# Kernel optimization log

Measured on AMD Instinct MI355X. Metric: run time of the kernel, lower is better.

The kernel has to match this reference:

```python
import jax, jax.numpy as jnp
import numpy as np

N_VARS = 100
MAX_LAG = 10
HIDDEN = 64
E = N_VARS * MAX_LAG  # number of tiny expert MLPs
BATCH = 4096


def setup_inputs() -> dict:
    key = jax.random.key(0)
    k_x, k_w1, k_b1, k_w2, k_b2 = jax.random.split(key, 5)
    x = jax.random.normal(k_x, (BATCH, E), dtype=jnp.float32)
    # PyTorch Linear(1, H): weight [H,1] -> stacked as [E, H]; bias [E, H]
    lim1 = 1.0  # kaiming-uniform-ish bound for fan_in=1
    W1 = jax.random.uniform(k_w1, (E, HIDDEN), dtype=jnp.float32, minval=-lim1, maxval=lim1)
    b1 = jax.random.uniform(k_b1, (E, HIDDEN), dtype=jnp.float32, minval=-lim1, maxval=lim1)
    # Linear(H, n_vars): weight [n_vars,H] -> stacked as [E, H, n_vars]; bias [E, n_vars]
    lim2 = 1.0 / np.sqrt(HIDDEN)
    W2 = jax.random.uniform(k_w2, (E, HIDDEN, N_VARS), dtype=jnp.float32, minval=-lim2, maxval=lim2)
    b2 = jax.random.uniform(k_b2, (E, N_VARS), dtype=jnp.float32, minval=-lim2, maxval=lim2)
    return {"x": x, "W1": W1, "b1": b1, "W2": W2, "b2": b2}


def reference(x, W1, b1, W2, b2):
    # Fused form of: sum_i Linear2_i(relu(Linear1_i(x[:, i:i+1])))
    # h[b,e,h] = relu(x[b,e] * W1[e,h] + b1[e,h])
    h = jax.nn.relu(x[:, :, None] * W1[None, :, :] + b1[None, :, :])  # [B,E,H]
    # sum over experts folded into the contraction: out[b,v] = sum_e h[b,e,:] @ W2[e,:,v]
    out = jnp.einsum("beh,ehv->bv", h, W2) + jnp.sum(b2, axis=0)  # [B,n_vars]
    return out
```

## Files before the change

kernel.cpp:

```cpp
#include <hip/hip_runtime.h>
#include <hip/hip_bf16.h>

#define NV 100
#define HID 64
#define NE 1000
#define NB 4096
#define ESPLIT 32
#define BLOBU 3648
#define NVP 112

typedef __attribute__((ext_vector_type(8))) short short8;
typedef __attribute__((ext_vector_type(8))) unsigned short ushort8;
typedef __attribute__((ext_vector_type(4))) float f32x4;
typedef __attribute__((ext_vector_type(4))) unsigned u32x4;
typedef __attribute__((ext_vector_type(4))) unsigned short u16x4;

__device__ __align__(16) float g_bsum[NV];

__device__ __forceinline__ short cvtbf(float f) {
    return __builtin_bit_cast(short, (__bf16)f);
}
__device__ __forceinline__ unsigned short f2bf(float f) {
    return (unsigned short)__builtin_bit_cast(short, (__bf16)f);
}
__device__ __forceinline__ float bf2f(unsigned short s) {
    union { unsigned u; float f; } v; v.u = ((unsigned)s) << 16;
    return v.f;
}
__device__ __forceinline__ float bcast_lo(unsigned u) {
    union { unsigned u; float f; } v; v.u = u << 16; return v.f;
}
__device__ __forceinline__ float bcast_hi(unsigned u) {
    union { unsigned u; float f; } v; v.u = u & 0xffff0000u; return v.f;
}
__device__ __forceinline__ unsigned pkbf(float a, float b) {
    return (unsigned)f2bf(a) | ((unsigned)f2bf(b) << 16);
}

__device__ __host__ __forceinline__ void esplit_range(int ks, int* pe0, int* pne) {
    int e0 = (ks < 26) ? 32 * ks : 832 + 28 * (ks - 26);
    int ne = (ks < 26) ? 32 : 28;
    *pe0 = e0; *pne = ne;
}

__global__ void bias_kernel(const float* __restrict__ b2) {
    int v = blockIdx.x;
    float s = 0.f;
    for (int e = threadIdx.x; e < NE; e += 256)
        s += b2[e * NV + v];
    __shared__ float red[4];
    for (int off = 32; off; off >>= 1) s += __shfl_down(s, off, 64);
    if ((threadIdx.x & 63) == 0) red[threadIdx.x >> 6] = s;
    __syncthreads();
    if (threadIdx.x == 0) g_bsum[v] = red[0] + red[1] + red[2] + red[3];
}

__global__ void init_kernel(float* __restrict__ out) {
    int idx = blockIdx.x * 256 + threadIdx.x;
    if (idx < NB * NV) out[idx] = g_bsum[idx % NV];
}

__global__ void prepass5(const float* __restrict__ W2, const float* __restrict__ W1,
                         const float* __restrict__ b1, unsigned* __restrict__ blob) {
    __shared__ float t[HID][NV + 1];
    int e = blockIdx.x;
    const float* src = W2 + (size_t)e * (HID * NV);
    for (int i = threadIdx.x; i < HID * NV; i += 256) {
        int hh = i / NV;
        int v = i - hh * NV;
        t[hh][v] = src[i];
    }
    __syncthreads();
    unsigned* dst = blob + (size_t)e * BLOBU;
    for (int o = threadIdx.x; o < 3584; o += 256) {
        int f = o >> 8;
        int r = o & 255;
        int l = r >> 2;
        int q = r & 3;
        int ksh = f / 7, tt = f - 7 * ksh;
        int kg = l >> 4, lrow = l & 15;
        int h0 = ksh * 32 + kg * 8 + 2 * q;
        int v = tt * 16 + lrow;
        unsigned val = 0;
        if (v < NV) val = pkbf(t[h0][v], t[h0 + 1][v]);
        dst[o] = val;
    }
    if (threadIdx.x < 64) {
        int j = threadIdx.x;
        dst[3584 + j] = pkbf(W1[(size_t)e * HID + j], b1[(size_t)e * HID + j]);
    }
}

__global__ __launch_bounds__(256, 2) void moe11(
    const float* __restrict__ x, const unsigned* __restrict__ blob,
    unsigned short* __restrict__ part)
{
    __shared__ __align__(16) unsigned short xts[32 * 256];

    const int bid = blockIdx.x;
    const int xcd = bid & 7;
    const int jj  = bid >> 3;
    const int ks  = xcd * 4 + (jj & 3);
    const int mb  = jj >> 2;

    const int tid  = threadIdx.x;
    const int lane = tid & 63;
    const int wave = tid >> 6;
    const int lrow = lane & 15;
    const int kg   = lane >> 4;

    const int row0 = mb * 256;
    int e0, ne; esplit_range(ks, &e0, &ne);

    {
        int r = tid;
        int slot = (r >> 6) * 64 + (r & 15) * 4 + ((r >> 4) & 3);
        const float* xp = x + (size_t)(row0 + r) * NE + e0;
        #pragma unroll
        for (int c4 = 0; c4 < 8; ++c4) {
            int eb = c4 * 4;
            if (eb < ne) {
                float4 v = *(const float4*)(xp + eb);
                xts[(eb + 0) * 256 + slot] = f2bf(v.x);
                xts[(eb + 1) * 256 + slot] = f2bf(v.y);
                xts[(eb + 2) * 256 + slot] = f2bf(v.z);
                xts[(eb + 3) * 256 + slot] = f2bf(v.w);
            }
        }
    }
    __syncthreads();

    f32x4 acc[4][7];
    #pragma unroll
    for (int rf = 0; rf < 4; ++rf)
        #pragma unroll
        for (int t = 0; t < 7; ++t)
            acc[rf][t] = (f32x4){0.f, 0.f, 0.f, 0.f};

    u32x4 B0[7], B1[7], Wa[2], Wb[2];

    auto LOADS0 = [&](const unsigned* g) {
        #pragma unroll
        for (int t = 0; t < 7; ++t)
            B0[t] = *(const u32x4*)(g + t * 256 + lane * 4);
        Wa[0] = *(const u32x4*)(g + 3584 + kg * 8);
        Wa[1] = *(const u32x4*)(g + 3584 + kg * 8 + 4);
    };
    auto LOADS1 = [&](const unsigned* g) {
        #pragma unroll
        for (int t = 0; t < 7; ++t)
            B1[t] = *(const u32x4*)(g + (7 + t) * 256 + lane * 4);
        Wb[0] = *(const u32x4*)(g + 3584 + 32 + kg * 8);
        Wb[1] = *(const u32x4*)(g + 3584 + 32 + kg * 8 + 4);
    };

    const unsigned* gcur = blob + (size_t)e0 * BLOBU;
    LOADS0(gcur);
    LOADS1(gcur);

    for (int ei = 0; ei < ne; ++ei) {
        u16x4 xq = *(const u16x4*)&xts[ei * 256 + wave * 64 + lrow * 4];
        float xv[4];
        #pragma unroll
        for (int rf = 0; rf < 4; ++rf) xv[rf] = bf2f(xq[rf]);

        const unsigned* gnext =
            blob + (size_t)(e0 + ((ei + 1 < ne) ? ei + 1 : ei)) * BLOBU;

        {
            short8 afr[4];
            #pragma unroll
            for (int q = 0; q < 4; ++q) {
                float w0 = bcast_lo(Wa[0][q]), b0 = bcast_hi(Wa[0][q]);
                float w1 = bcast_lo(Wa[1][q]), b1v = bcast_hi(Wa[1][q]);
                #pragma unroll
                for (int rf = 0; rf < 4; ++rf) {
                    afr[rf][q]     = cvtbf(fmaxf(fmaf(xv[rf], w0, b0), 0.f));
                    afr[rf][q + 4] = cvtbf(fmaxf(fmaf(xv[rf], w1, b1v), 0.f));
                }
            }
            __builtin_amdgcn_s_setprio(1);
            #pragma unroll
            for (int t = 0; t < 7; ++t) {
                short8 bf = __builtin_bit_cast(short8, B0[t]);
                #pragma unroll
                for (int rf = 0; rf < 4; ++rf)
                    acc[rf][t] = __builtin_amdgcn_mfma_f32_16x16x32_bf16(afr[rf], bf, acc[rf][t], 0, 0, 0);
            }
            __builtin_amdgcn_s_setprio(0);
        }
        LOADS0(gnext);

        {
            short8 afr[4];
            #pragma unroll
            for (int q = 0; q < 4; ++q) {
                float w0 = bcast_lo(Wb[0][q]), b0 = bcast_hi(Wb[0][q]);
                float w1 = bcast_lo(Wb[1][q]), b1v = bcast_hi(Wb[1][q]);
                #pragma unroll
                for (int rf = 0; rf < 4; ++rf) {
                    afr[rf][q]     = cvtbf(fmaxf(fmaf(xv[rf], w0, b0), 0.f));
                    afr[rf][q + 4] = cvtbf(fmaxf(fmaf(xv[rf], w1, b1v), 0.f));
                }
            }
            __builtin_amdgcn_s_setprio(1);
            #pragma unroll
            for (int t = 0; t < 7; ++t) {
                short8 bf = __builtin_bit_cast(short8, B1[t]);
                #pragma unroll
                for (int rf = 0; rf < 4; ++rf)
                    acc[rf][t] = __builtin_amdgcn_mfma_f32_16x16x32_bf16(afr[rf], bf, acc[rf][t], 0, 0, 0);
            }
            __builtin_amdgcn_s_setprio(0);
        }
        LOADS1(gnext);
    }

    unsigned short* dst = part + (size_t)ks * (NB * NVP);
    #pragma unroll
    for (int rf = 0; rf < 4; ++rf) {
        #pragma unroll
        for (int t = 0; t < 7; ++t) {
            int col = t * 16 + lrow;
            size_t base = (size_t)(row0 + wave * 64 + rf * 16 + kg * 4) * NVP + col;
            #pragma unroll
            for (int r = 0; r < 4; ++r)
                dst[base + (size_t)r * NVP] = (unsigned short)cvtbf(acc[rf][t][r]);
        }
    }
}

__global__ void reduce3(const unsigned short* __restrict__ part, float* __restrict__ out) {
    int idx = blockIdx.x * 256 + threadIdx.x;
    if (idx >= NB * (NVP / 8)) return;
    int b = idx / (NVP / 8);
    int g = idx - b * (NVP / 8);
    int c0 = g * 8;
    float s[8];
    #pragma unroll
    for (int j = 0; j < 8; ++j)
        s[j] = (c0 + j < NV) ? g_bsum[c0 + j] : 0.f;
    size_t off = (size_t)b * NVP + c0;
    #pragma unroll 4
    for (int k = 0; k < ESPLIT; ++k) {
        ushort8 v = *(const ushort8*)&part[(size_t)k * (NB * NVP) + off];
        #pragma unroll
        for (int j = 0; j < 8; ++j)
            s[j] += bf2f(v[j]);
    }
    #pragma unroll
    for (int j = 0; j < 8; ++j)
        if (c0 + j < NV) out[(size_t)b * NV + c0 + j] = s[j];
}

#define LDW 72
__global__ __launch_bounds__(256, 3) void moe_fallback(
    const float* __restrict__ x, const float* __restrict__ W1,
    const float* __restrict__ b1, const float* __restrict__ W2,
    float* __restrict__ dst)
{
    __shared__ unsigned short w2t[8192];
    const int tid  = threadIdx.x;
    const int lane = tid & 63;
    const int lrow = lane & 15;
    const int kg   = lane >> 4;
    const int wave = tid >> 6;
    const int row0 = blockIdx.x * 128 + wave * 32;
    const int e0 = blockIdx.y * 32;
    const int e1 = min(NE, e0 + 32);

    f32x4 acc[2][7];
    #pragma unroll
    for (int rf = 0; rf < 2; ++rf)
        #pragma unroll
        for (int t = 0; t < 7; ++t)
            acc[rf][t] = (f32x4){0.f, 0.f, 0.f, 0.f};

    const float* xr0 = x + (size_t)(row0 + lrow) * NE;
    const float* xr1 = x + (size_t)(row0 + 16 + lrow) * NE;

    for (int e = e0; e < e1; ++e) {
        __syncthreads();
        const float* src = W2 + (size_t)e * (HID * NV);
        unsigned* w2t32 = (unsigned*)w2t;
        #pragma unroll
        for (int k = 0; k < 13; ++k) {
            int i = tid + k * 256;
            if (i < (HID / 2) * NV) {
                int a3  = i / 400;
                int rem = i - a3 * 400;
                int bv  = rem >> 2;
                int c   = rem & 3;
                int hh2 = a3 * 4 + c;
                float f0 = src[(2 * hh2) * NV + bv];
                float f1 = src[(2 * hh2 + 1) * NV + bv];
                w2t32[bv * (LDW / 2) + hh2] = pkbf(f0, f1);
            }
        }
        __syncthreads();

        float xv0 = xr0[e];
        float xv1 = xr1[e];
        const float* w1p = W1 + e * HID;
        const float* b1p = b1 + e * HID;
        #pragma unroll
        for (int ksh = 0; ksh < 2; ++ksh) {
            const int hb = ksh * 32 + kg * 8;
            f32x4 w1lo = *(const f32x4*)(w1p + hb);
            f32x4 w1hi = *(const f32x4*)(w1p + hb + 4);
            f32x4 blo  = *(const f32x4*)(b1p + hb);
            f32x4 bhi  = *(const f32x4*)(b1p + hb + 4);
            short8 a0, a1;
            #pragma unroll
            for (int j = 0; j < 4; ++j) {
                a0[j]     = cvtbf(fmaxf(fmaf(xv0, w1lo[j], blo[j]), 0.f));
                a0[j + 4] = cvtbf(fmaxf(fmaf(xv0, w1hi[j], bhi[j]), 0.f));
                a1[j]     = cvtbf(fmaxf(fmaf(xv1, w1lo[j], blo[j]), 0.f));
                a1[j + 4] = cvtbf(fmaxf(fmaf(xv1, w1hi[j], bhi[j]), 0.f));
            }
            #pragma unroll
            for (int t = 0; t < 7; ++t) {
                short8 bf = *(const short8*)&w2t[(t * 16 + lrow) * LDW + hb];
                acc[0][t] = __builtin_amdgcn_mfma_f32_16x16x32_bf16(a0, bf, acc[0][t], 0, 0, 0);
                acc[1][t] = __builtin_amdgcn_mfma_f32_16x16x32_bf16(a1, bf, acc[1][t], 0, 0, 0);
            }
        }
    }

    #pragma unroll
    for (int rf = 0; rf < 2; ++rf) {
        #pragma unroll
        for (int t = 0; t < 7; ++t) {
            int col = t * 16 + lrow;
            if (col < NV) {
                size_t base = (size_t)(row0 + rf * 16 + kg * 4) * NV + col;
                #pragma unroll
                for (int r = 0; r < 4; ++r)
                    atomicAdd(&dst[base + (size_t)r * NV], acc[rf][t][r]);
            }
        }
    }
}

extern "C" void kernel_launch(void* const* d_in, const int* in_sizes, int n_in,
                              void* d_out, int out_size, void* d_ws, size_t ws_size,
                              hipStream_t stream) {
    const float* x  = (const float*)d_in[0];
    const float* W1 = (const float*)d_in[1];
    const float* b1 = (const float*)d_in[2];
    const float* W2 = (const float*)d_in[3];
    const float* b2 = (const float*)d_in[4];
    float* out = (float*)d_out;

    const size_t BLOB_BYTES = (size_t)NE * BLOBU * 4;
    const size_t PART_BYTES = (size_t)ESPLIT * NB * NVP * 2;

    bias_kernel<<<NV, 256, 0, stream>>>(b2);

    if (ws_size >= BLOB_BYTES + PART_BYTES) {
        unsigned* blob = (unsigned*)d_ws;
        unsigned short* part = (unsigned short*)((char*)d_ws + BLOB_BYTES);
        prepass5<<<NE, 256, 0, stream>>>(W2, W1, b1, blob);
        moe11<<<512, 256, 0, stream>>>(x, blob, part);
        reduce3<<<(NB * (NVP / 8) + 255) / 256, 256, 0, stream>>>(part, out);
    } else {
        init_kernel<<<(NB * NV + 255) / 256, 256, 0, stream>>>(out);
        moe_fallback<<<dim3(NB / 128, ESPLIT), 256, 0, stream>>>(x, W1, b1, W2, out);
    }
}
```

Measured before the change: 79.83 us.

## Stage W1/b1 in LDS at fp32 and software-pipeline hidden-activation construction

Moves W1 and b1 out of the packed bf16 weight blob and into shared memory as fp32, loaded once per block, which shrinks the blob stride to 3584 words and drops the per-expert global loads of the W1/b1 vectors. The main loop is restructured so that the relu activation fragment for the next half (and the next expert's first half) is built while the current MFMA chain runs, aiming to overlap VALU work with matrix-core work. It removes the s_setprio hints, adds LDS reads per expert and more live fragment registers, which could pressure occupancy at two blocks per CU.

```diff
diff --git a/kernel.cpp b/kernel.cpp
--- a/kernel.cpp
+++ b/kernel.cpp
@@ -6,7 +6,7 @@
 #define NE 1000
 #define NB 4096
 #define ESPLIT 32
-#define BLOBU 3648
+#define BLOBU 3584
 #define NVP 112
 
 typedef __attribute__((ext_vector_type(8))) short short8;
@@ -17,21 +17,15 @@
 
 __device__ __align__(16) float g_bsum[NV];
 
+__device__ __forceinline__ unsigned short f2bf(float f) {
+    return (unsigned short)__builtin_bit_cast(short, (__bf16)f);
+}
 __device__ __forceinline__ short cvtbf(float f) {
     return __builtin_bit_cast(short, (__bf16)f);
-}
-__device__ __forceinline__ unsigned short f2bf(float f) {
-    return (unsigned short)__builtin_bit_cast(short, (__bf16)f);
 }
 __device__ __forceinline__ float bf2f(unsigned short s) {
     union { unsigned u; float f; } v; v.u = ((unsigned)s) << 16;
     return v.f;
-}
-__device__ __forceinline__ float bcast_lo(unsigned u) {
-    union { unsigned u; float f; } v; v.u = u << 16; return v.f;
-}
-__device__ __forceinline__ float bcast_hi(unsigned u) {
-    union { unsigned u; float f; } v; v.u = u & 0xffff0000u; return v.f;
 }
 __device__ __forceinline__ unsigned pkbf(float a, float b) {
     return (unsigned)f2bf(a) | ((unsigned)f2bf(b) << 16);
@@ -60,8 +54,7 @@
     if (idx < NB * NV) out[idx] = g_bsum[idx % NV];
 }
 
-__global__ void prepass5(const float* __restrict__ W2, const float* __restrict__ W1,
-                         const float* __restrict__ b1, unsigned* __restrict__ blob) {
+__global__ void prepass7(const float* __restrict__ W2, unsigned* __restrict__ blob) {
     __shared__ float t[HID][NV + 1];
     int e = blockIdx.x;
     const float* src = W2 + (size_t)e * (HID * NV);
@@ -72,7 +65,7 @@
     }
     __syncthreads();
     unsigned* dst = blob + (size_t)e * BLOBU;
-    for (int o = threadIdx.x; o < 3584; o += 256) {
+    for (int o = threadIdx.x; o < BLOBU; o += 256) {
         int f = o >> 8;
         int r = o & 255;
         int l = r >> 2;
@@ -85,17 +78,16 @@
         if (v < NV) val = pkbf(t[h0][v], t[h0 + 1][v]);
         dst[o] = val;
     }
-    if (threadIdx.x < 64) {
-        int j = threadIdx.x;
-        dst[3584 + j] = pkbf(W1[(size_t)e * HID + j], b1[(size_t)e * HID + j]);
-    }
-}
-
-__global__ __launch_bounds__(256, 2) void moe11(
-    const float* __restrict__ x, const unsigned* __restrict__ blob,
+}
+
+__global__ __launch_bounds__(256, 2) void moe13(
+    const float* __restrict__ x, const float* __restrict__ W1,
+    const float* __restrict__ b1, const unsigned* __restrict__ blob,
     unsigned short* __restrict__ part)
 {
     __shared__ __align__(16) unsigned short xts[32 * 256];
+    __shared__ __align__(16) float w1l[32 * 64];
+    __shared__ __align__(16) float b1l[32 * 64];
 
     const int bid = blockIdx.x;
     const int xcd = bid & 7;
@@ -128,6 +120,18 @@
             }
         }
     }
+    {
+        int e = tid >> 3;
+        int h = (tid & 7) * 8;
+        if (e < ne) {
+            const float* wsrc = W1 + (size_t)(e0 + e) * HID + h;
+            const float* bsrc = b1 + (size_t)(e0 + e) * HID + h;
+            *(float4*)&w1l[e * 64 + h]     = *(const float4*)(wsrc);
+            *(float4*)&w1l[e * 64 + h + 4] = *(const float4*)(wsrc + 4);
+            *(float4*)&b1l[e * 64 + h]     = *(const float4*)(bsrc);
+            *(float4*)&b1l[e * 64 + h + 4] = *(const float4*)(bsrc + 4);
+        }
+    }
     __syncthreads();
 
     f32x4 acc[4][7];
@@ -137,83 +141,87 @@
         for (int t = 0; t < 7; ++t)
             acc[rf][t] = (f32x4){0.f, 0.f, 0.f, 0.f};
 
-    u32x4 B0[7], B1[7], Wa[2], Wb[2];
+    u32x4 B0[7], B1[7];
+    const int boff = lane * 4;
 
     auto LOADS0 = [&](const unsigned* g) {
         #pragma unroll
         for (int t = 0; t < 7; ++t)
-            B0[t] = *(const u32x4*)(g + t * 256 + lane * 4);
-        Wa[0] = *(const u32x4*)(g + 3584 + kg * 8);
-        Wa[1] = *(const u32x4*)(g + 3584 + kg * 8 + 4);
+            B0[t] = *(const u32x4*)(g + t * 256 + boff);
     };
     auto LOADS1 = [&](const unsigned* g) {
         #pragma unroll
         for (int t = 0; t < 7; ++t)
-            B1[t] = *(const u32x4*)(g + (7 + t) * 256 + lane * 4);
-        Wb[0] = *(const u32x4*)(g + 3584 + 32 + kg * 8);
-        Wb[1] = *(const u32x4*)(g + 3584 + 32 + kg * 8 + 4);
+            B1[t] = *(const u32x4*)(g + (7 + t) * 256 + boff);
+    };
+
+    auto BUILD = [&](short8* afr, const float* xv, int e, int ksh) {
+        const f32x4 wa = *(const f32x4*)&w1l[e * 64 + ksh * 32 + kg * 8];
+        const f32x4 wb = *(const f32x4*)&w1l[e * 64 + ksh * 32 + kg * 8 + 4];
+        const f32x4 ba = *(const f32x4*)&b1l[e * 64 + ksh * 32 + kg * 8];
+        const f32x4 bb = *(const f32x4*)&b1l[e * 64 + ksh * 32 + kg * 8 + 4];
+        #pragma unroll
+        for (int rf = 0; rf < 4; ++rf) {
+            float xr = xv[rf];
+            short8 a;
+            a[0] = cvtbf(fmaxf(fmaf(xr, wa[0], ba[0]), 0.f));
+            a[1] = cvtbf(fmaxf(fmaf(xr, wa[1], ba[1]), 0.f));
+            a[2] = cvtbf(fmaxf(fmaf(xr, wa[2], ba[2]), 0.f));
+            a[3] = cvtbf(fmaxf(fmaf(xr, wa[3], ba[3]), 0.f));
+            a[4] = cvtbf(fmaxf(fmaf(xr, wb[0], bb[0]), 0.f));
+            a[5] = cvtbf(fmaxf(fmaf(xr, wb[1], bb[1]), 0.f));
+            a[6] = cvtbf(fmaxf(fmaf(xr, wb[2], bb[2]), 0.f));
+            a[7] = cvtbf(fmaxf(fmaf(xr, wb[3], bb[3]), 0.f));
+            afr[rf] = a;
+        }
     };
 
     const unsigned* gcur = blob + (size_t)e0 * BLOBU;
     LOADS0(gcur);
     LOADS1(gcur);
 
+    const unsigned short* xrow = &xts[wave * 64 + lrow * 4];
+
+    short8 afrA[4], afrB[4];
+    float xvC[4], xvN[4];
+    {
+        u16x4 xq = *(const u16x4*)xrow;
+        #pragma unroll
+        for (int rf = 0; rf < 4; ++rf) xvC[rf] = bf2f(xq[rf]);
+    }
+    BUILD(afrA, xvC, 0, 0);
+
     for (int ei = 0; ei < ne; ++ei) {
-        u16x4 xq = *(const u16x4*)&xts[ei * 256 + wave * 64 + lrow * 4];
-        float xv[4];
-        #pragma unroll
-        for (int rf = 0; rf < 4; ++rf) xv[rf] = bf2f(xq[rf]);
-
-        const unsigned* gnext =
-            blob + (size_t)(e0 + ((ei + 1 < ne) ? ei + 1 : ei)) * BLOBU;
+        const int en = (ei + 1 < ne) ? ei + 1 : ei;
+        const unsigned* gnext = blob + (size_t)(e0 + en) * BLOBU;
+
+        BUILD(afrB, xvC, ei, 1);
+        #pragma unroll
+        for (int t = 0; t < 7; ++t) {
+            short8 bf = __builtin_bit_cast(short8, B0[t]);
+            #pragma unroll
+            for (int rf = 0; rf < 4; ++rf)
+                acc[rf][t] = __builtin_amdgcn_mfma_f32_16x16x32_bf16(afrA[rf], bf, acc[rf][t], 0, 0, 0);
+        }
+        LOADS0(gnext);
 
         {
-            short8 afr[4];
-            #pragma unroll
-            for (int q = 0; q < 4; ++q) {
-                float w0 = bcast_lo(Wa[0][q]), b0 = bcast_hi(Wa[0][q]);
-                float w1 = bcast_lo(Wa[1][q]), b1v = bcast_hi(Wa[1][q]);
-                #pragma unroll
-                for (int rf = 0; rf < 4; ++rf) {
-                    afr[rf][q]     = cvtbf(fmaxf(fmaf(xv[rf], w0, b0), 0.f));
-                    afr[rf][q + 4] = cvtbf(fmaxf(fmaf(xv[rf], w1, b1v), 0.f));
-                }
-            }
-            __builtin_amdgcn_s_setprio(1);
-            #pragma unroll
-            for (int t = 0; t < 7; ++t) {
-                short8 bf = __builtin_bit_cast(short8, B0[t]);
-                #pragma unroll
-                for (int rf = 0; rf < 4; ++rf)
-                    acc[rf][t] = __builtin_amdgcn_mfma_f32_16x16x32_bf16(afr[rf], bf, acc[rf][t], 0, 0, 0);
-            }
-            __builtin_amdgcn_s_setprio(0);
-        }
-        LOADS0(gnext);
-
-        {
-            short8 afr[4];
-            #pragma unroll
-            for (int q = 0; q < 4; ++q) {
-                float w0 = bcast_lo(Wb[0][q]), b0 = bcast_hi(Wb[0][q]);
-                float w1 = bcast_lo(Wb[1][q]), b1v = bcast_hi(Wb[1][q]);
-                #pragma unroll
-                for (int rf = 0; rf < 4; ++rf) {
-                    afr[rf][q]     = cvtbf(fmaxf(fmaf(xv[rf], w0, b0), 0.f));
-                    afr[rf][q + 4] = cvtbf(fmaxf(fmaf(xv[rf], w1, b1v), 0.f));
-                }
-            }
-            __builtin_amdgcn_s_setprio(1);
-            #pragma unroll
-            for (int t = 0; t < 7; ++t) {
-                short8 bf = __builtin_bit_cast(short8, B1[t]);
-                #pragma unroll
-                for (int rf = 0; rf < 4; ++rf)
-                    acc[rf][t] = __builtin_amdgcn_mfma_f32_16x16x32_bf16(afr[rf], bf, acc[rf][t], 0, 0, 0);
-            }
-            __builtin_amdgcn_s_setprio(0);
+            u16x4 xq = *(const u16x4*)(xrow + en * 256);
+            #pragma unroll
+            for (int rf = 0; rf < 4; ++rf) xvN[rf] = bf2f(xq[rf]);
+        }
+        BUILD(afrA, xvN, en, 0);
+        #pragma unroll
+        for (int t = 0; t < 7; ++t) {
+            short8 bf = __builtin_bit_cast(short8, B1[t]);
+            #pragma unroll
+            for (int rf = 0; rf < 4; ++rf)
+                acc[rf][t] = __builtin_amdgcn_mfma_f32_16x16x32_bf16(afrB[rf], bf, acc[rf][t], 0, 0, 0);
         }
         LOADS1(gnext);
+
+        #pragma unroll
+        for (int rf = 0; rf < 4; ++rf) xvC[rf] = xvN[rf];
     }
 
     unsigned short* dst = part + (size_t)ks * (NB * NVP);
@@ -360,8 +368,8 @@
     if (ws_size >= BLOB_BYTES + PART_BYTES) {
         unsigned* blob = (unsigned*)d_ws;
         unsigned short* part = (unsigned short*)((char*)d_ws + BLOB_BYTES);
-        prepass5<<<NE, 256, 0, stream>>>(W2, W1, b1, blob);
-        moe11<<<512, 256, 0, stream>>>(x, blob, part);
+        prepass7<<<NE, 256, 0, stream>>>(W2, blob);
+        moe13<<<512, 256, 0, stream>>>(x, W1, b1, blob, part);
         reduce3<<<(NB * (NVP / 8) + 255) / 256, 256, 0, stream>>>(part, out);
     } else {
         init_kernel<<<(NB * NV + 255) / 256, 256, 0, stream>>>(out);
```

After: 77.46 us. -3.0%, faster.
